# Kernel tuning notes

Measured on AMD Instinct MI355X. Metric: run time of the kernel, lower is better.

Reference implementation:

```python
import jax, jax.numpy as jnp
import numpy as np

ALIGNED_H = 7
ALIGNED_W = 7
IMG_H, IMG_W = 800.0, 1216.0


def setup_inputs() -> dict:
    key = jax.random.key(0)
    k1, k2, k3, k4 = jax.random.split(key, 4)
    N, C, H, W = 2, 256, 200, 304
    R = 2000
    features = jax.random.normal(k1, (N, C, H, W), dtype=jnp.float32)
    # rois: [batch_idx, x1, y1, x2, y2] in image coordinates
    bidx = jax.random.randint(k2, (R,), 0, N).astype(jnp.float32)
    xy1 = jax.random.uniform(k3, (R, 2)) * jnp.array([IMG_W * 0.7, IMG_H * 0.7])
    wh = 16.0 + jax.random.uniform(k4, (R, 2)) * jnp.array([IMG_W * 0.3 - 16.0, IMG_H * 0.3 - 16.0])
    xy2 = jnp.minimum(xy1 + wh, jnp.array([IMG_W - 1.0, IMG_H - 1.0]))
    rois = jnp.concatenate([bidx[:, None], xy1[:, 0:1], xy1[:, 1:2], xy2[:, 0:1], xy2[:, 1:2]], axis=1).astype(jnp.float32)
    spatial_scale = jnp.float32(0.25)
    return {"features": features, "rois": rois, "spatial_scale": spatial_scale}


def roi_align(features, rois, spatial_scale, ah, aw):
    N, C, H, W = features.shape
    b = rois[:, 0].astype(jnp.int32)                       # [R]
    x1 = rois[:, 1] * spatial_scale
    y1 = rois[:, 2] * spatial_scale
    x2 = rois[:, 3] * spatial_scale
    y2 = rois[:, 4] * spatial_scale
    roi_w = jnp.maximum(x2 - x1 + 1.0, 0.0)
    roi_h = jnp.maximum(y2 - y1 + 1.0, 0.0)
    bin_h = roi_h / (ah - 1.0)                             # [R]
    bin_w = roi_w / (aw - 1.0)
    ph = jnp.arange(ah, dtype=jnp.float32)
    pw = jnp.arange(aw, dtype=jnp.float32)
    h = y1[:, None] + ph[None, :] * bin_h[:, None]         # [R, ah]
    w = x1[:, None] + pw[None, :] * bin_w[:, None]         # [R, aw]
    valid = ((h >= 0) & (h < H))[:, :, None] & ((w >= 0) & (w < W))[:, None, :]  # [R, ah, aw]
    hs = jnp.clip(jnp.floor(h), 0.0, H - 2.0)              # kernel: min(floor(h), H-2)
    ws = jnp.clip(jnp.floor(w), 0.0, W - 2.0)
    dh = (h - hs)[:, :, None]                              # [R, ah, 1]
    dw = (w - ws)[:, None, :]                              # [R, 1, aw]
    yi = hs.astype(jnp.int32)[:, :, None]                  # [R, ah, 1]
    xi = ws.astype(jnp.int32)[:, None, :]                  # [R, 1, aw]
    bi = b[:, None, None]                                  # [R, 1, 1]
    # gather 4 corners -> [R, ah, aw, C]
    v00 = features[bi, :, yi, xi]
    v01 = features[bi, :, yi, xi + 1]
    v10 = features[bi, :, yi + 1, xi]
    v11 = features[bi, :, yi + 1, xi + 1]
    dh4 = dh[..., None]
    dw4 = dw[..., None]
    val = (v00 * (1 - dh4) * (1 - dw4) + v01 * (1 - dh4) * dw4
           + v10 * dh4 * (1 - dw4) + v11 * dh4 * dw4)
    out = jnp.where(valid[..., None], val, 0.0)            # [R, ah, aw, C]
    return jnp.transpose(out, (0, 3, 1, 2))                # [R, C, ah, aw]


def reference(features, rois, spatial_scale):
    return roi_align(features, rois, spatial_scale, ALIGNED_H, ALIGNED_W)
```

## Files before the change

kernel.cpp:

```cpp
#include <hip/hip_runtime.h>

#define C_ 256
#define H_ 200
#define W_ 304
#define AH 7
#define AW 7
#define KK 49
#define PADK 66

typedef float f32x4  __attribute__((ext_vector_type(4)));
typedef float f32x4u __attribute__((ext_vector_type(4), aligned(4)));

__device__ __forceinline__ float h2f(unsigned short s) {
    _Float16 h; __builtin_memcpy(&h, &s, 2); return (float)h;
}
__device__ __forceinline__ unsigned short f2h(float f) {
    _Float16 h = (_Float16)f; unsigned short s; __builtin_memcpy(&s, &h, 2); return s;
}

__global__ __launch_bounds__(256) void transpose_nchw_nhwc_f16(
    const float* __restrict__ in, unsigned short* __restrict__ out) {
    __shared__ unsigned int tile[128][34];
    const int HW = H_ * W_;
    const int n  = blockIdx.z;
    const int p0 = blockIdx.x * 64;
    const int c0 = blockIdx.y * 128;
    const float* inb = in + (size_t)n * C_ * HW;
    unsigned short* outb = out + (size_t)n * HW * C_;

    {
        const int q  = threadIdx.x & 15;
        const int r0 = threadIdx.x >> 4;
        #pragma unroll
        for (int i = 0; i < 8; ++i) {
            const int c = r0 + 16 * i;
            const f32x4 v = __builtin_nontemporal_load(
                (const f32x4*)&inb[(size_t)(c0 + c) * HW + p0 + 4 * q]);
            const unsigned int ulo = (unsigned)f2h(v.x) | ((unsigned)f2h(v.y) << 16);
            const unsigned int uhi = (unsigned)f2h(v.z) | ((unsigned)f2h(v.w) << 16);
            *(uint2*)&tile[c][2 * q] = make_uint2(ulo, uhi);
        }
    }
    __syncthreads();
    {
        const int pp0 = threadIdx.x & 15;
        const int cq  = threadIdx.x >> 4;
        #pragma unroll
        for (int i = 0; i < 2; ++i) {
            const int pp = pp0 + 16 * i;
            unsigned int u[8];
            #pragma unroll
            for (int jj = 0; jj < 8; ++jj) u[jj] = tile[8 * cq + jj][pp];
            unsigned int pe[4], po[4];
            #pragma unroll
            for (int k = 0; k < 4; ++k) {
                pe[k] = (u[2 * k] & 0xFFFFu) | (u[2 * k + 1] << 16);
                po[k] = (u[2 * k] >> 16) | (u[2 * k + 1] & 0xFFFF0000u);
            }
            unsigned short* oA = &outb[(size_t)(p0 + 2 * pp) * C_ + c0 + 8 * cq];
            unsigned short* oB = oA + C_;
            *(uint4*)oA = make_uint4(pe[0], pe[1], pe[2], pe[3]);
            *(uint4*)oB = make_uint4(po[0], po[1], po[2], po[3]);
        }
    }
}

__device__ __forceinline__ void samp(
    const unsigned short* __restrict__ fb, int k,
    float y1, float x1, float bin_h, float bin_w, int c4, float* o) {
    const int ph = k / AW;
    const int pw = k - ph * AW;
    const float h  = y1 + (float)ph * bin_h;
    const float w  = x1 + (float)pw * bin_w;
    const float hs = fminf(fmaxf(floorf(h), 0.0f), (float)(H_ - 2));
    const float ws = fminf(fmaxf(floorf(w), 0.0f), (float)(W_ - 2));
    const float dh = h - hs;
    const float dw = w - ws;
    const int   yi = (int)hs;
    const int   xi = (int)ws;
    const bool  valid = (h >= 0.0f) && (h < (float)H_) &&
                        (w >= 0.0f) && (w < (float)W_);
    const unsigned short* p = fb + ((size_t)yi * W_ + xi) * C_ + c4;
    const ushort4 a00 = *(const ushort4*)p;
    const ushort4 a01 = *(const ushort4*)(p + C_);
    const ushort4 a10 = *(const ushort4*)(p + (size_t)W_ * C_);
    const ushort4 a11 = *(const ushort4*)(p + (size_t)W_ * C_ + C_);
    const float w00 = (1.0f - dh) * (1.0f - dw);
    const float w01 = (1.0f - dh) * dw;
    const float w10 = dh * (1.0f - dw);
    const float w11 = dh * dw;
    o[0] = h2f(a00.x) * w00 + h2f(a01.x) * w01 + h2f(a10.x) * w10 + h2f(a11.x) * w11;
    o[1] = h2f(a00.y) * w00 + h2f(a01.y) * w01 + h2f(a10.y) * w10 + h2f(a11.y) * w11;
    o[2] = h2f(a00.z) * w00 + h2f(a01.z) * w01 + h2f(a10.z) * w10 + h2f(a11.z) * w11;
    o[3] = h2f(a00.w) * w00 + h2f(a01.w) * w01 + h2f(a10.w) * w10 + h2f(a11.w) * w11;
    if (!valid) { o[0] = 0.0f; o[1] = 0.0f; o[2] = 0.0f; o[3] = 0.0f; }
}

__global__ __launch_bounds__(512, 6) void roialign_nhwc_f16(
    const unsigned short* __restrict__ tf, const float* __restrict__ rois,
    const float* __restrict__ scale_ptr, float* __restrict__ out) {
    __shared__ unsigned short sh[C_ * PADK];
    const int r    = blockIdx.x;
    const int wave = threadIdx.x >> 6;
    const int lane = threadIdx.x & 63;
    const int c4   = lane * 4;

    const float scale = scale_ptr[0];
    const float* roi = rois + (size_t)r * 5;
    const int   b  = (int)roi[0];
    const float x1 = roi[1] * scale;
    const float y1 = roi[2] * scale;
    const float x2 = roi[3] * scale;
    const float y2 = roi[4] * scale;
    const float roi_w = fmaxf(x2 - x1 + 1.0f, 0.0f);
    const float roi_h = fmaxf(y2 - y1 + 1.0f, 0.0f);
    const float bin_h = roi_h / (float)(AH - 1);
    const float bin_w = roi_w / (float)(AW - 1);
    const unsigned short* fb = tf + (size_t)b * (H_ * W_) * C_;

    for (int kp = 3 * wave; kp < 3 * wave + 3; ++kp) {
        const int kA = 2 * kp;
        float vA[4], vB[4];
        samp(fb, kA,     y1, x1, bin_h, bin_w, c4, vA);
        samp(fb, kA + 1, y1, x1, bin_h, bin_w, c4, vB);
        #pragma unroll
        for (int j = 0; j < 4; ++j) {
            const unsigned int u = (unsigned)f2h(vA[j]) | ((unsigned)f2h(vB[j]) << 16);
            *(unsigned int*)&sh[(c4 + j) * PADK + kA] = u;
        }
    }
    if (wave == 7) {
        float v[4];
        samp(fb, 48, y1, x1, bin_h, bin_w, c4, v);
        #pragma unroll
        for (int j = 0; j < 4; ++j) sh[(c4 + j) * PADK + 48] = f2h(v[j]);
    }
    __syncthreads();

    const int j  = threadIdx.x & 7;
    const int cs = threadIdx.x >> 3;
    float* ob = out + (size_t)r * (C_ * KK);
    if (j < 7) {
        #pragma unroll
        for (int it = 0; it < 4; ++it) {
            const int c = cs + 64 * it;
            const unsigned short* row = &sh[c * PADK + 8 * j];
            float f[8];
            #pragma unroll
            for (int e = 0; e < 4; ++e) {
                const unsigned int u = *(const unsigned int*)&row[2 * e];
                f[2 * e]     = h2f((unsigned short)(u & 0xFFFFu));
                f[2 * e + 1] = h2f((unsigned short)(u >> 16));
            }
            float* dst = &ob[c * KK + 8 * j];
            if (j < 6) {
                f32x4u a = { f[0], f[1], f[2], f[3] };
                f32x4u bb = { f[4], f[5], f[6], f[7] };
                __builtin_nontemporal_store(a, (f32x4u*)dst);
                __builtin_nontemporal_store(bb, (f32x4u*)(dst + 4));
            } else {
                __builtin_nontemporal_store(f[0], dst);
            }
        }
    }
}

__global__ __launch_bounds__(256) void roialign_nchw(
    const float* __restrict__ feat, const float* __restrict__ rois,
    const float* __restrict__ scale_ptr, float* __restrict__ out) {
    __shared__ float sout[C_ * KK];
    const int r = blockIdx.x;
    const int c = threadIdx.x;
    const float scale = scale_ptr[0];
    const float* roi = rois + (size_t)r * 5;
    const int   b  = (int)roi[0];
    const float x1 = roi[1] * scale;
    const float y1 = roi[2] * scale;
    const float x2 = roi[3] * scale;
    const float y2 = roi[4] * scale;
    const float roi_w = fmaxf(x2 - x1 + 1.0f, 0.0f);
    const float roi_h = fmaxf(y2 - y1 + 1.0f, 0.0f);
    const float bin_h = roi_h / (float)(AH - 1);
    const float bin_w = roi_w / (float)(AW - 1);
    const float* fb = feat + ((size_t)b * C_ + c) * (H_ * W_);

    for (int ph = 0; ph < AH; ++ph) {
        const float h  = y1 + (float)ph * bin_h;
        const float hs = fminf(fmaxf(floorf(h), 0.0f), (float)(H_ - 2));
        const float dh = h - hs;
        const int   yi = (int)hs;
        const bool  vh = (h >= 0.0f) && (h < (float)H_);
        #pragma unroll
        for (int pw = 0; pw < AW; ++pw) {
            const float w  = x1 + (float)pw * bin_w;
            const float ws = fminf(fmaxf(floorf(w), 0.0f), (float)(W_ - 2));
            const float dw = w - ws;
            const int   xi = (int)ws;
            const bool  valid = vh && (w >= 0.0f) && (w < (float)W_);
            const float v00 = fb[(size_t)yi * W_ + xi];
            const float v01 = fb[(size_t)yi * W_ + xi + 1];
            const float v10 = fb[(size_t)(yi + 1) * W_ + xi];
            const float v11 = fb[(size_t)(yi + 1) * W_ + xi + 1];
            float val = v00 * (1.0f - dh) * (1.0f - dw)
                      + v01 * (1.0f - dh) * dw
                      + v10 * dh * (1.0f - dw)
                      + v11 * dh * dw;
            sout[c * KK + ph * AW + pw] = valid ? val : 0.0f;
        }
    }
    __syncthreads();
    float* ob = out + (size_t)r * C_ * KK;
    #pragma unroll 4
    for (int i = threadIdx.x; i < C_ * KK; i += 256) ob[i] = sout[i];
}

extern "C" void kernel_launch(void* const* d_in, const int* in_sizes, int n_in,
                              void* d_out, int out_size, void* d_ws, size_t ws_size,
                              hipStream_t stream) {
    const float* feat  = (const float*)d_in[0];
    const float* rois  = (const float*)d_in[1];
    const float* scale = (const float*)d_in[2];
    float* out = (float*)d_out;

    const int R = in_sizes[1] / 5;
    const int N = in_sizes[0] / (C_ * H_ * W_);
    const size_t need = (size_t)N * C_ * H_ * W_ * sizeof(unsigned short);

    if (ws_size >= need) {
        unsigned short* tf = (unsigned short*)d_ws;
        dim3 tb(256);
        dim3 tg((H_ * W_) / 64, C_ / 128, N);
        hipLaunchKernelGGL(transpose_nchw_nhwc_f16, tg, tb, 0, stream, feat, tf);
        hipLaunchKernelGGL(roialign_nhwc_f16, dim3(R), dim3(512), 0, stream,
                           tf, rois, scale, out);
    } else {
        hipLaunchKernelGGL(roialign_nchw, dim3(R), dim3(256), 0, stream,
                           feat, rois, scale, out);
    }
}
```

Before: 94.43 us.

## Restructure ROIAlign LDS layout to sample-major with coalesced scalar output stores

Changes the shared-memory staging buffer from channel-major with padded halves to a sample-major layout of packed half pairs, so each wave writes one sample point per iteration over a strided loop instead of paired samples. The write-out phase becomes a flat, fully coalesced loop where each thread stores one float per step using divide/modulo indexing, replacing the 8-wide vector stores that left one of every eight lanes idle. It also drops the occupancy hint from the launch bounds. This trades wide vector stores for scalar stores and extra integer division in exchange for perfect coalescing and simpler bank-conflict behavior.

```diff
diff --git a/kernel.cpp b/kernel.cpp
--- a/kernel.cpp
+++ b/kernel.cpp
@@ -6,10 +6,9 @@
 #define AH 7
 #define AW 7
 #define KK 49
-#define PADK 66
-
-typedef float f32x4  __attribute__((ext_vector_type(4)));
-typedef float f32x4u __attribute__((ext_vector_type(4), aligned(4)));
+#define ROWU 131
+
+typedef float f32x4 __attribute__((ext_vector_type(4)));
 
 __device__ __forceinline__ float h2f(unsigned short s) {
     _Float16 h; __builtin_memcpy(&h, &s, 2); return (float)h;
@@ -96,10 +95,10 @@
     if (!valid) { o[0] = 0.0f; o[1] = 0.0f; o[2] = 0.0f; o[3] = 0.0f; }
 }
 
-__global__ __launch_bounds__(512, 6) void roialign_nhwc_f16(
+__global__ __launch_bounds__(512) void roialign_nhwc_f16(
     const unsigned short* __restrict__ tf, const float* __restrict__ rois,
     const float* __restrict__ scale_ptr, float* __restrict__ out) {
-    __shared__ unsigned short sh[C_ * PADK];
+    __shared__ unsigned int shu[KK * ROWU];
     const int r    = blockIdx.x;
     const int wave = threadIdx.x >> 6;
     const int lane = threadIdx.x & 63;
@@ -118,49 +117,28 @@
     const float bin_w = roi_w / (float)(AW - 1);
     const unsigned short* fb = tf + (size_t)b * (H_ * W_) * C_;
 
-    for (int kp = 3 * wave; kp < 3 * wave + 3; ++kp) {
-        const int kA = 2 * kp;
-        float vA[4], vB[4];
-        samp(fb, kA,     y1, x1, bin_h, bin_w, c4, vA);
-        samp(fb, kA + 1, y1, x1, bin_h, bin_w, c4, vB);
-        #pragma unroll
-        for (int j = 0; j < 4; ++j) {
-            const unsigned int u = (unsigned)f2h(vA[j]) | ((unsigned)f2h(vB[j]) << 16);
-            *(unsigned int*)&sh[(c4 + j) * PADK + kA] = u;
-        }
-    }
-    if (wave == 7) {
+    #pragma unroll 2
+    for (int k = wave; k < KK; k += 8) {
         float v[4];
-        samp(fb, 48, y1, x1, bin_h, bin_w, c4, v);
-        #pragma unroll
-        for (int j = 0; j < 4; ++j) sh[(c4 + j) * PADK + 48] = f2h(v[j]);
+        samp(fb, k, y1, x1, bin_h, bin_w, c4, v);
+        const unsigned int u0 = (unsigned)f2h(v[0]) | ((unsigned)f2h(v[1]) << 16);
+        const unsigned int u1 = (unsigned)f2h(v[2]) | ((unsigned)f2h(v[3]) << 16);
+        shu[k * ROWU + 2 * lane]     = u0;
+        shu[k * ROWU + 2 * lane + 1] = u1;
     }
     __syncthreads();
 
-    const int j  = threadIdx.x & 7;
-    const int cs = threadIdx.x >> 3;
     float* ob = out + (size_t)r * (C_ * KK);
-    if (j < 7) {
-        #pragma unroll
-        for (int it = 0; it < 4; ++it) {
-            const int c = cs + 64 * it;
-            const unsigned short* row = &sh[c * PADK + 8 * j];
-            float f[8];
-            #pragma unroll
-            for (int e = 0; e < 4; ++e) {
-                const unsigned int u = *(const unsigned int*)&row[2 * e];
-                f[2 * e]     = h2f((unsigned short)(u & 0xFFFFu));
-                f[2 * e + 1] = h2f((unsigned short)(u >> 16));
-            }
-            float* dst = &ob[c * KK + 8 * j];
-            if (j < 6) {
-                f32x4u a = { f[0], f[1], f[2], f[3] };
-                f32x4u bb = { f[4], f[5], f[6], f[7] };
-                __builtin_nontemporal_store(a, (f32x4u*)dst);
-                __builtin_nontemporal_store(bb, (f32x4u*)(dst + 4));
-            } else {
-                __builtin_nontemporal_store(f[0], dst);
-            }
+    #pragma unroll
+    for (int i = 0; i < 25; ++i) {
+        const int f = threadIdx.x + 512 * i;
+        if (i < 24 || f < C_ * KK) {
+            const int c = f / KK;
+            const int k = f - c * KK;
+            const unsigned int u = shu[k * ROWU + (c >> 1)];
+            const unsigned short hv = (c & 1) ? (unsigned short)(u >> 16)
+                                              : (unsigned short)(u & 0xFFFFu);
+            __builtin_nontemporal_store(h2f(hv), &ob[f]);
         }
     }
 }
```

Measured after the change: 78.96 us, median of 2. 16.4% less time.
